# Kernel tuning notes

Hardware: AMD Instinct MI355X
Metric: run time of the kernel (lower is better)

## Reference

```python
import jax, jax.numpy as jnp
import numpy as np

FILTERS = 256
KH, KW = 3, 3
SH, SW = 1, 1
IN_CH = 128


def setup_inputs() -> dict:
    key = jax.random.key(0)
    k1, k2 = jax.random.split(key)
    inputs = jax.random.normal(k1, (32, 112, 112, IN_CH), dtype=jnp.float32)
    # Glorot-uniform init matching the layer's build()
    limit = np.sqrt(6.0 / (KH * KW * IN_CH + FILTERS)).astype(np.float32)
    kernel = jax.random.uniform(k2, (KH, KW, IN_CH, FILTERS), dtype=jnp.float32,
                                minval=-limit, maxval=limit)
    bias = jnp.zeros((FILTERS,), dtype=jnp.float32)
    return {"inputs": inputs, "kernel": kernel, "bias": bias}


def reference(inputs, kernel, bias):
    # Equivalent math to extract_patches(SAME) + flattened matmul + bias:
    # a standard 2D convolution in NHWC with HWIO kernel.
    out = jax.lax.conv_general_dilated(
        inputs, kernel,
        window_strides=(SH, SW),
        padding="SAME",
        dimension_numbers=("NHWC", "HWIO", "NHWC"),
    )
    return out + bias
```

## Files before the change

### kernel.cpp

```cpp
#include <hip/hip_runtime.h>

typedef __attribute__((ext_vector_type(4))) float   floatx4;
typedef __attribute__((ext_vector_type(8))) __bf16  bf16x8;
typedef unsigned short ushort_t;
typedef __attribute__((ext_vector_type(8))) ushort_t ushortx8;

typedef const unsigned int __attribute__((address_space(1)))* gptr_t;
typedef unsigned int __attribute__((address_space(3)))* lptr_t;

#define NIMG 32
#define H    112
#define W    112
#define CIN  128
#define COUT 256
#define HP   114
#define WP   114
#define HW   12544

#define BM 256
#define BN 256
#define BK 64
#define NT 18

__device__ __forceinline__ ushort_t f32_to_bf16(float f) {
    unsigned u = __float_as_uint(f);
    unsigned r = 0x7fffu + ((u >> 16) & 1u);
    return (ushort_t)((u + r) >> 16);
}

__global__ __launch_bounds__(256) void prepad_input(const float* __restrict__ in,
                                                    ushort_t* __restrict__ pad) {
    int t   = blockIdx.x * 256 + threadIdx.x;
    int ic8 = t & 15;
    int sp  = t >> 4;
    int iw  = sp % WP;
    int sp2 = sp / WP;
    int ih  = sp2 % HP;
    int n   = sp2 / HP;
    ushortx8 v;
    if (ih >= 1 && ih <= H && iw >= 1 && iw <= W) {
        const float* src = in + ((size_t)((n * H + (ih - 1)) * W + (iw - 1))) * CIN + ic8 * 8;
        floatx4 a = *reinterpret_cast<const floatx4*>(src);
        floatx4 b = *reinterpret_cast<const floatx4*>(src + 4);
#pragma unroll
        for (int j = 0; j < 4; ++j) { v[j] = f32_to_bf16(a[j]); v[4 + j] = f32_to_bf16(b[j]); }
    } else {
#pragma unroll
        for (int j = 0; j < 8; ++j) v[j] = 0;
    }
    reinterpret_cast<ushortx8*>(pad)[t] = v;
}

__global__ __launch_bounds__(256) void wtrans(const float* __restrict__ k,
                                              ushort_t* __restrict__ wt) {
    int t    = blockIdx.x * 256 + threadIdx.x;
    int ic   = t & 127;
    int oc   = (t >> 7) & 255;
    int khkw = t >> 15;
    wt[t] = f32_to_bf16(k[((size_t)(khkw * CIN + ic)) * COUT + oc]);
}


__device__ __forceinline__ int aoffK(int t) {
    int tap = t >> 1;
    return ((tap / 3) * WP + (tap % 3)) * CIN + (t & 1) * 64;
}
__device__ __forceinline__ int boffK(int t) {
    int tap = t >> 1;
    return tap * (COUT * CIN) + (t & 1) * 64;
}

__global__ __launch_bounds__(512, 2) void conv_mfma8(const ushort_t* __restrict__ pad,
                                                     const ushort_t* __restrict__ wt,
                                                     const float* __restrict__ bias,
                                                     float* __restrict__ out) {
    __shared__ __align__(16) ushort_t lds[65536];

    const int tid  = threadIdx.x;
    const int wid  = tid >> 6;
    const int lane = tid & 63;
    const int wm   = wid >> 2;
    const int wn   = wid & 3;
    const int bid  = blockIdx.x;
    const int bm   = (bid & 7) * 196 + (bid >> 3);

    const int trow = tid >> 3;
    const int lc   = (tid & 7) ^ (trow & 7);

    const ushort_t* srcA[4];
    const ushort_t* srcB[4];
#pragma unroll
    for (int i = 0; i < 4; ++i) {
        int m  = bm * BM + i * 64 + trow;
        int n  = m / HW;
        int r  = m % HW;
        int oh = r / W;
        int ow = r % W;
        srcA[i] = pad + ((size_t)((n * HP + oh) * WP + ow)) * CIN + lc * 8;
        int oc = i * 64 + trow;
        srcB[i] = wt + (size_t)oc * CIN + lc * 8;
    }
    const int dstSlot = wid * 512;

#define STAGE_A(tile, half)                                                                         \
    { int _o = aoffK(tile); int _b = ((tile) & 1) * 32768 + (half) * 8192 + dstSlot;                \
      __builtin_amdgcn_global_load_lds((gptr_t)(srcA[(half)*2+0] + _o), (lptr_t)&lds[_b       ], 16, 0, 0); \
      __builtin_amdgcn_global_load_lds((gptr_t)(srcA[(half)*2+1] + _o), (lptr_t)&lds[_b + 4096], 16, 0, 0); }
#define STAGE_B(tile, half)                                                                         \
    { int _o = boffK(tile); int _b = ((tile) & 1) * 32768 + 16384 + (half) * 8192 + dstSlot;        \
      __builtin_amdgcn_global_load_lds((gptr_t)(srcB[(half)*2+0] + _o), (lptr_t)&lds[_b       ], 16, 0, 0); \
      __builtin_amdgcn_global_load_lds((gptr_t)(srcB[(half)*2+1] + _o), (lptr_t)&lds[_b + 4096], 16, 0, 0); }

    const int aBase = wm * 8192 + (lane & 15) * 64;
    const int bBase = 16384 + (wn >> 1) * 8192 + ((wn & 1) * 64 + (lane & 15)) * 64;
    int cOff[2];
#pragma unroll
    for (int ks = 0; ks < 2; ++ks)
        cOff[ks] = ((ks * 4 + (lane >> 4)) ^ (lane & 7)) * 8;

    floatx4 acc[8][4];
#pragma unroll
    for (int i = 0; i < 8; ++i)
#pragma unroll
        for (int j = 0; j < 4; ++j) acc[i][j] = (floatx4)0.0f;

    STAGE_A(0, 0); STAGE_A(0, 1); STAGE_B(0, 0); STAGE_B(0, 1);
    STAGE_B(1, 0); STAGE_B(1, 1);
    asm volatile("s_waitcnt vmcnt(4)" ::: "memory");
    __builtin_amdgcn_s_barrier();

    for (int t = 0; t < NT; ++t) {
        const int bufb = (t & 1) * 32768;
        bf16x8 bfr[4][2];
#pragma unroll
        for (int q = 0; q < 4; ++q) {
            bf16x8 af[2][2];
#pragma unroll
            for (int rfl = 0; rfl < 2; ++rfl)
#pragma unroll
                for (int ks = 0; ks < 2; ++ks)
                    af[rfl][ks] = *reinterpret_cast<const bf16x8*>(&lds[bufb + aBase + (2 * q + rfl) * 1024 + cOff[ks]]);
            if (q == 0) {
#pragma unroll
                for (int cf = 0; cf < 2; ++cf)
#pragma unroll
                    for (int ks = 0; ks < 2; ++ks)
                        bfr[cf][ks] = *reinterpret_cast<const bf16x8*>(&lds[bufb + bBase + cf * 1024 + cOff[ks]]);
            }
            if (q == 0 && t + 1 < NT) STAGE_A(t + 1, 0);
            if (q == 1 && t + 1 < NT) STAGE_A(t + 1, 1);
            if (q == 2 && t + 2 < NT) STAGE_B(t + 2, 0);
            if (q == 3 && t + 2 < NT) STAGE_B(t + 2, 1);
            __builtin_amdgcn_s_barrier();
            __builtin_amdgcn_s_setprio(1);
            if (q == 0) {
#pragma unroll
                for (int rfl = 0; rfl < 2; ++rfl)
#pragma unroll
                    for (int cf = 0; cf < 2; ++cf)
#pragma unroll
                        for (int ks = 0; ks < 2; ++ks)
                            acc[rfl][cf] = __builtin_amdgcn_mfma_f32_16x16x32_bf16(
                                af[rfl][ks], bfr[cf][ks], acc[rfl][cf], 0, 0, 0);
#pragma unroll
                for (int cf = 2; cf < 4; ++cf)
#pragma unroll
                    for (int ks = 0; ks < 2; ++ks)
                        bfr[cf][ks] = *reinterpret_cast<const bf16x8*>(&lds[bufb + bBase + cf * 1024 + cOff[ks]]);
#pragma unroll
                for (int rfl = 0; rfl < 2; ++rfl)
#pragma unroll
                    for (int cf = 2; cf < 4; ++cf)
#pragma unroll
                        for (int ks = 0; ks < 2; ++ks)
                            acc[rfl][cf] = __builtin_amdgcn_mfma_f32_16x16x32_bf16(
                                af[rfl][ks], bfr[cf][ks], acc[rfl][cf], 0, 0, 0);
            } else {
#pragma unroll
                for (int rfl = 0; rfl < 2; ++rfl)
#pragma unroll
                    for (int cf = 0; cf < 4; ++cf)
#pragma unroll
                        for (int ks = 0; ks < 2; ++ks)
                            acc[2 * q + rfl][cf] = __builtin_amdgcn_mfma_f32_16x16x32_bf16(
                                af[rfl][ks], bfr[cf][ks], acc[2 * q + rfl][cf], 0, 0, 0);
            }
            __builtin_amdgcn_s_setprio(0);
            if (q == 3) {
                if (t < NT - 2)       { asm volatile("s_waitcnt vmcnt(4)" ::: "memory"); }
                else if (t == NT - 2) { asm volatile("s_waitcnt vmcnt(0)" ::: "memory"); }
            }
            __builtin_amdgcn_s_barrier();
        }
    }

    const int col0 = wn * 64 + (lane & 15);
    const int row0 = bm * BM + wm * 128 + (lane >> 4) * 4;
    float bv[4];
#pragma unroll
    for (int cf = 0; cf < 4; ++cf) bv[cf] = bias[col0 + cf * 16];
#pragma unroll
    for (int rf = 0; rf < 8; ++rf)
#pragma unroll
        for (int cf = 0; cf < 4; ++cf)
#pragma unroll
            for (int r = 0; r < 4; ++r)
                out[(size_t)(row0 + rf * 16 + r) * COUT + col0 + cf * 16] = acc[rf][cf][r] + bv[cf];
#undef STAGE_A
#undef STAGE_B
}

extern "C" void kernel_launch(void* const* d_in, const int* in_sizes, int n_in,
                              void* d_out, int out_size, void* d_ws, size_t ws_size,
                              hipStream_t stream) {
    const float* input = (const float*)d_in[0];
    const float* kern  = (const float*)d_in[1];
    const float* bias  = (const float*)d_in[2];
    float* out         = (float*)d_out;

    ushort_t* pad = (ushort_t*)d_ws;
    ushort_t* wt  = pad + (size_t)NIMG * HP * WP * CIN;

    prepad_input<<<25992, 256, 0, stream>>>(input, pad);
    wtrans<<<1152, 256, 0, stream>>>(kern, wt);
    conv_mfma8<<<1568, 512, 0, stream>>>(pad, wt, bias, out);
}
```

Before: 362.3 us.

## Fuse input padding and bf16 conversion into conv kernel A-tile loads

Removes the separate prepad kernel that wrote a padded bf16 copy of the input. The conv kernel now loads fp32 input directly into registers, masks out-of-bounds taps with precomputed per-row validity bits, converts to bf16 and writes to LDS, interleaved with the MFMA pipeline. This saves a full read/write pass over the activations and one kernel launch. In exchange, the A operand now moves as fp32 through registers instead of direct global-to-LDS loads, doubling A-side global traffic inside the main loop and adding VGPR pressure and extra waits.

```diff
diff --git a/kernel.cpp b/kernel.cpp
--- a/kernel.cpp
+++ b/kernel.cpp
@@ -13,8 +13,6 @@
 #define W    112
 #define CIN  128
 #define COUT 256
-#define HP   114
-#define WP   114
 #define HW   12544
 
 #define BM 256
@@ -28,27 +26,14 @@
     return (ushort_t)((u + r) >> 16);
 }
 
-__global__ __launch_bounds__(256) void prepad_input(const float* __restrict__ in,
-                                                    ushort_t* __restrict__ pad) {
-    int t   = blockIdx.x * 256 + threadIdx.x;
-    int ic8 = t & 15;
-    int sp  = t >> 4;
-    int iw  = sp % WP;
-    int sp2 = sp / WP;
-    int ih  = sp2 % HP;
-    int n   = sp2 / HP;
-    ushortx8 v;
-    if (ih >= 1 && ih <= H && iw >= 1 && iw <= W) {
-        const float* src = in + ((size_t)((n * H + (ih - 1)) * W + (iw - 1))) * CIN + ic8 * 8;
-        floatx4 a = *reinterpret_cast<const floatx4*>(src);
-        floatx4 b = *reinterpret_cast<const floatx4*>(src + 4);
-#pragma unroll
-        for (int j = 0; j < 4; ++j) { v[j] = f32_to_bf16(a[j]); v[4 + j] = f32_to_bf16(b[j]); }
-    } else {
-#pragma unroll
-        for (int j = 0; j < 8; ++j) v[j] = 0;
-    }
-    reinterpret_cast<ushortx8*>(pad)[t] = v;
+__device__ __forceinline__ ushortx8 cvt_sel(floatx4 a, floatx4 b, bool v) {
+    ushortx8 o;
+#pragma unroll
+    for (int j = 0; j < 4; ++j) {
+        o[j]     = v ? f32_to_bf16(a[j]) : (ushort_t)0;
+        o[4 + j] = v ? f32_to_bf16(b[j]) : (ushort_t)0;
+    }
+    return o;
 }
 
 __global__ __launch_bounds__(256) void wtrans(const float* __restrict__ k,
@@ -60,17 +45,13 @@
     wt[t] = f32_to_bf16(k[((size_t)(khkw * CIN + ic)) * COUT + oc]);
 }
 
-
-__device__ __forceinline__ int aoffK(int t) {
-    int tap = t >> 1;
-    return ((tap / 3) * WP + (tap % 3)) * CIN + (t & 1) * 64;
-}
 __device__ __forceinline__ int boffK(int t) {
     int tap = t >> 1;
     return tap * (COUT * CIN) + (t & 1) * 64;
 }
 
-__global__ __launch_bounds__(512, 2) void conv_mfma8(const ushort_t* __restrict__ pad,
+
+__global__ __launch_bounds__(512, 2) void conv_mfma8(const float* __restrict__ in,
                                                      const ushort_t* __restrict__ wt,
                                                      const float* __restrict__ bias,
                                                      float* __restrict__ out) {
@@ -87,7 +68,8 @@
     const int trow = tid >> 3;
     const int lc   = (tid & 7) ^ (trow & 7);
 
-    const ushort_t* srcA[4];
+    int offA[4];
+    int vbits[4];
     const ushort_t* srcB[4];
 #pragma unroll
     for (int i = 0; i < 4; ++i) {
@@ -96,21 +78,33 @@
         int r  = m % HW;
         int oh = r / W;
         int ow = r % W;
-        srcA[i] = pad + ((size_t)((n * HP + oh) * WP + ow)) * CIN + lc * 8;
-        int oc = i * 64 + trow;
-        srcB[i] = wt + (size_t)oc * CIN + lc * 8;
+        offA[i] = ((n * H + oh) * W + ow) * CIN + lc * 8;
+        int vb = 0;
+#pragma unroll
+        for (int tap = 0; tap < 9; ++tap) {
+            int kh = tap / 3, kw = tap - 3 * (tap / 3);
+            if ((unsigned)(oh + kh - 1) < (unsigned)H && (unsigned)(ow + kw - 1) < (unsigned)W)
+                vb |= (1 << tap);
+        }
+        vbits[i] = vb;
+        srcB[i] = wt + (size_t)(i * 64 + trow) * CIN + lc * 8;
     }
     const int dstSlot = wid * 512;
 
-#define STAGE_A(tile, half)                                                                         \
-    { int _o = aoffK(tile); int _b = ((tile) & 1) * 32768 + (half) * 8192 + dstSlot;                \
-      __builtin_amdgcn_global_load_lds((gptr_t)(srcA[(half)*2+0] + _o), (lptr_t)&lds[_b       ], 16, 0, 0); \
-      __builtin_amdgcn_global_load_lds((gptr_t)(srcA[(half)*2+1] + _o), (lptr_t)&lds[_b + 4096], 16, 0, 0); }
 #define STAGE_B(tile, half)                                                                         \
     { int _o = boffK(tile); int _b = ((tile) & 1) * 32768 + 16384 + (half) * 8192 + dstSlot;        \
       __builtin_amdgcn_global_load_lds((gptr_t)(srcB[(half)*2+0] + _o), (lptr_t)&lds[_b       ], 16, 0, 0); \
       __builtin_amdgcn_global_load_lds((gptr_t)(srcB[(half)*2+1] + _o), (lptr_t)&lds[_b + 4096], 16, 0, 0); }
 
+#define LOAD_A(s, offF, tapi)                                                                       \
+    { bool _v = (vbits[s] >> (tapi)) & 1;                                                           \
+      const float* _p = in + (ptrdiff_t)(offA[s] + (_v ? (offF) : 0));                              \
+      fa0[s] = *reinterpret_cast<const floatx4*>(_p);                                               \
+      fa1[s] = *reinterpret_cast<const floatx4*>(_p + 4); }
+#define WRITE_A(s, bufn, tapi)                                                                      \
+    { bool _v = (vbits[s] >> (tapi)) & 1;                                                           \
+      *reinterpret_cast<ushortx8*>(&lds[(bufn) + (s) * 4096 + tid * 8]) = cvt_sel(fa0[s], fa1[s], _v); }
+
     const int aBase = wm * 8192 + (lane & 15) * 64;
     const int bBase = 16384 + (wn >> 1) * 8192 + ((wn & 1) * 64 + (lane & 15)) * 64;
     int cOff[2];
@@ -124,13 +118,30 @@
 #pragma unroll
         for (int j = 0; j < 4; ++j) acc[i][j] = (floatx4)0.0f;
 
-    STAGE_A(0, 0); STAGE_A(0, 1); STAGE_B(0, 0); STAGE_B(0, 1);
-    STAGE_B(1, 0); STAGE_B(1, 1);
-    asm volatile("s_waitcnt vmcnt(4)" ::: "memory");
-    __builtin_amdgcn_s_barrier();
+    floatx4 fa0[4], fa1[4];
+
+    {
+        const int offF0 = ((0 - 1) * W + (0 - 1)) * CIN;
+        LOAD_A(0, offF0, 0); LOAD_A(1, offF0, 0);
+        asm volatile("s_waitcnt vmcnt(0)" ::: "memory");
+        WRITE_A(0, 0, 0); WRITE_A(1, 0, 0);
+        LOAD_A(2, offF0, 0); LOAD_A(3, offF0, 0);
+        STAGE_B(0, 0); STAGE_B(0, 1);
+        STAGE_B(1, 0); STAGE_B(1, 1);
+        asm volatile("s_waitcnt vmcnt(8)" ::: "memory");
+        WRITE_A(2, 0, 0); WRITE_A(3, 0, 0);
+        asm volatile("s_waitcnt vmcnt(4)" ::: "memory");
+        asm volatile("s_waitcnt lgkmcnt(0)" ::: "memory");
+        __builtin_amdgcn_s_barrier();
+    }
 
     for (int t = 0; t < NT; ++t) {
         const int bufb = (t & 1) * 32768;
+        const int bufn = ((t + 1) & 1) * 32768;
+        const int tap1  = (t + 1) >> 1;
+        const int kh1   = tap1 / 3;
+        const int kw1   = tap1 - 3 * kh1;
+        const int offF1 = ((kh1 - 1) * W + (kw1 - 1)) * CIN + ((t + 1) & 1) * 64;
         bf16x8 bfr[4][2];
 #pragma unroll
         for (int q = 0; q < 4; ++q) {
@@ -147,8 +158,7 @@
                     for (int ks = 0; ks < 2; ++ks)
                         bfr[cf][ks] = *reinterpret_cast<const bf16x8*>(&lds[bufb + bBase + cf * 1024 + cOff[ks]]);
             }
-            if (q == 0 && t + 1 < NT) STAGE_A(t + 1, 0);
-            if (q == 1 && t + 1 < NT) STAGE_A(t + 1, 1);
+            if (q == 0 && t + 1 < NT) { LOAD_A(0, offF1, tap1); LOAD_A(1, offF1, tap1); }
             if (q == 2 && t + 2 < NT) STAGE_B(t + 2, 0);
             if (q == 3 && t + 2 < NT) STAGE_B(t + 2, 1);
             __builtin_amdgcn_s_barrier();
@@ -186,10 +196,17 @@
                                 af[rfl][ks], bfr[cf][ks], acc[2 * q + rfl][cf], 0, 0, 0);
             }
             __builtin_amdgcn_s_setprio(0);
-            if (q == 3) {
-                if (t < NT - 2)       { asm volatile("s_waitcnt vmcnt(4)" ::: "memory"); }
-                else if (t == NT - 2) { asm volatile("s_waitcnt vmcnt(0)" ::: "memory"); }
-            }
+            if (q == 1 && t + 1 < NT) {
+                asm volatile("s_waitcnt vmcnt(0)" ::: "memory");
+                WRITE_A(0, bufn, tap1); WRITE_A(1, bufn, tap1);
+                LOAD_A(2, offF1, tap1); LOAD_A(3, offF1, tap1);
+            }
+            if (q == 2 && t + 1 < NT) {
+                if (t < NT - 2) { asm volatile("s_waitcnt vmcnt(2)" ::: "memory"); }
+                else            { asm volatile("s_waitcnt vmcnt(0)" ::: "memory"); }
+                WRITE_A(2, bufn, tap1); WRITE_A(3, bufn, tap1);
+            }
+            if (q == 3) { asm volatile("s_waitcnt lgkmcnt(0)" ::: "memory"); }
             __builtin_amdgcn_s_barrier();
         }
     }
@@ -206,8 +223,9 @@
 #pragma unroll
             for (int r = 0; r < 4; ++r)
                 out[(size_t)(row0 + rf * 16 + r) * COUT + col0 + cf * 16] = acc[rf][cf][r] + bv[cf];
-#undef STAGE_A
 #undef STAGE_B
+#undef LOAD_A
+#undef WRITE_A
 }
 
 extern "C" void kernel_launch(void* const* d_in, const int* in_sizes, int n_in,
@@ -218,10 +236,8 @@
     const float* bias  = (const float*)d_in[2];
     float* out         = (float*)d_out;
 
-    ushort_t* pad = (ushort_t*)d_ws;
-    ushort_t* wt  = pad + (size_t)NIMG * HP * WP * CIN;
-
-    prepad_input<<<25992, 256, 0, stream>>>(input, pad);
+    ushort_t* wt = (ushort_t*)d_ws;
+
     wtrans<<<1152, 256, 0, stream>>>(kern, wt);
-    conv_mfma8<<<1568, 512, 0, stream>>>(pad, wt, bias, out);
-}
+    conv_mfma8<<<1568, 512, 0, stream>>>(input, wt, bias, out);
+}
```

New measurement: 396.3 us. +9.4%, slower.
